# Kernel tuning notes

Measured on AMD Instinct MI355X. Metric: run time of the kernel, lower is better.

## Reference

```python
import jax, jax.numpy as jnp
import numpy as np

TEMPERATURE = 0.07
NEG = -9e15  # matches torch masked_fill value
EPS = 1e-8   # torch.nn.functional.cosine_similarity eps


def setup_inputs() -> dict:
    key = jax.random.key(0)
    k1, k2 = jax.random.split(key)
    B, D = 4096, 512
    return {
        "feats1": jax.random.normal(k1, (B, D), dtype=jnp.float32),
        "feats2": jax.random.normal(k2, (B, D), dtype=jnp.float32),
    }


def reference(feats1, feats2):
    feats = jnp.concatenate([feats1, feats2], axis=0)            # [2N, D]
    n = feats.shape[0]
    # cosine similarity via normalize-once + GEMM (same math as the
    # broadcasted F.cosine_similarity, incl. per-vector eps clamp)
    norms = jnp.maximum(jnp.linalg.norm(feats, axis=-1, keepdims=True), EPS)
    fn = feats / norms                                            # [2N, D]
    cos_sim = fn @ fn.T                                           # [2N, 2N]
    # mask self-similarity BEFORE temperature division (as in torch code)
    idx = jnp.arange(n)
    cos_sim = jnp.where(idx[:, None] == idx[None, :], NEG, cos_sim)
    cos_sim = cos_sim / TEMPERATURE
    # positive pair: eye rolled by N rows -> column (i + N) mod 2N
    pos_idx = (idx + n // 2) % n
    pos = cos_sim[idx, pos_idx]                                   # [2N]
    nll = jnp.mean(-pos + jax.nn.logsumexp(cos_sim, axis=-1))
    # ranking: rank of the positive among [pos, masked negatives];
    # equals # of masked entries strictly greater than pos
    masked = jnp.where(idx[None, :] == pos_idx[:, None], NEG, cos_sim)
    rank = jnp.sum(masked > pos[:, None], axis=-1)                # int [2N]
    acc_top1 = jnp.mean((rank == 0).astype(jnp.float32))
    acc_top5 = jnp.mean((rank < 5).astype(jnp.float32))
    acc_mean_pos = 1.0 + jnp.mean(rank.astype(jnp.float32))
    return (nll, acc_top1, acc_top5, acc_mean_pos)
```

## Files before the change

kernel.cpp:

```cpp
#include <hip/hip_runtime.h>
#include <math.h>
#include <stdint.h>

#define NTOT   8192
#define HALF_N 4096
#define DIM    512
#define INV_T  14.2857142857142857f
#define NTILE  64
#define NBLK   2080

using s16x8 = __attribute__((ext_vector_type(8))) short;
using f32x4 = __attribute__((ext_vector_type(4))) float;

__device__ unsigned short g_fnb[NTOT * DIM];
__device__ float g_pos[NTOT];
__device__ float g_ps[NTILE * NTOT];
__device__ int   g_pc[NTILE * NTOT];
__device__ float g_sumexp[NTOT];
__device__ int   g_cnt[NTOT];

__device__ __forceinline__ float bf2f(unsigned short u) {
  union { unsigned int i; float f; } v; v.i = ((unsigned int)u) << 16; return v.f;
}
__device__ __forceinline__ unsigned short f2bf(float x) {
  union { float f; unsigned int i; } v; v.f = x;
  unsigned int u = v.i;
  return (unsigned short)((u + 0x7FFFu + ((u >> 16) & 1u)) >> 16);
}

__device__ __forceinline__ void gload16(const unsigned short* g, unsigned short* l) {
  __builtin_amdgcn_global_load_lds(
      (const __attribute__((address_space(1))) unsigned int*)g,
      (__attribute__((address_space(3))) unsigned int*)l, 16, 0, 0);
}

__global__ __launch_bounds__(256) void knorm(const float* __restrict__ f1,
                                             const float* __restrict__ f2) {
  const int tid  = threadIdx.x;
  const int wv   = tid >> 6;
  const int pi   = wv >> 1;
  const int half = wv & 1;
  const int lane = tid & 63;
  const int b    = blockIdx.x * 2 + pi;
  const int row  = b + half * HALF_N;

  const float* src = (half == 0) ? (f1 + (size_t)b * DIM) : (f2 + (size_t)b * DIM);
  float4 v0 = ((const float4*)src)[lane];
  float4 v1 = ((const float4*)src)[lane + 64];
  float ss = v0.x*v0.x + v0.y*v0.y + v0.z*v0.z + v0.w*v0.w
           + v1.x*v1.x + v1.y*v1.y + v1.z*v1.z + v1.w*v1.w;
  #pragma unroll
  for (int o = 32; o >= 1; o >>= 1) ss += __shfl_xor(ss, o, 64);
  const float sc = 1.0f / fmaxf(sqrtf(ss), 1e-8f);
  ushort4 h0, h1;
  h0.x = f2bf(v0.x * sc); h0.y = f2bf(v0.y * sc);
  h0.z = f2bf(v0.z * sc); h0.w = f2bf(v0.w * sc);
  h1.x = f2bf(v1.x * sc); h1.y = f2bf(v1.y * sc);
  h1.z = f2bf(v1.z * sc); h1.w = f2bf(v1.w * sc);
  ushort4* dst = (ushort4*)(g_fnb + (size_t)row * DIM);
  dst[lane]      = h0;
  dst[lane + 64] = h1;

  __shared__ ushort4 sh[2][64][2];
  if (half == 1) { sh[pi][lane][0] = h0; sh[pi][lane][1] = h1; }
  __syncthreads();
  if (half == 0) {
    const ushort4 p0 = sh[pi][lane][0], p1 = sh[pi][lane][1];
    float s = bf2f(h0.x)*bf2f(p0.x) + bf2f(h0.y)*bf2f(p0.y)
            + bf2f(h0.z)*bf2f(p0.z) + bf2f(h0.w)*bf2f(p0.w)
            + bf2f(h1.x)*bf2f(p1.x) + bf2f(h1.y)*bf2f(p1.y)
            + bf2f(h1.z)*bf2f(p1.z) + bf2f(h1.w)*bf2f(p1.w);
    #pragma unroll
    for (int o = 32; o >= 1; o >>= 1) s += __shfl_xor(s, o, 64);
    if (lane == 0) { g_pos[b] = s; g_pos[b + HALF_N] = s; }
  }
}

__global__ __launch_bounds__(256, 4) void kmain() {
  __shared__ __align__(16) unsigned short As[128 * 64];
  __shared__ __align__(16) unsigned short Bs[128 * 64];
  __shared__ float sRowS[128]; __shared__ int sRowC[128];
  __shared__ float sColS[128]; __shared__ int sColC[128];

  int t = (blockIdx.x & 7) * (NBLK / 8) + (blockIdx.x >> 3);
  int bi = 0, rem = NTILE;
  while (t >= rem) { t -= rem; --rem; ++bi; }
  const int bj = bi + t;
  const bool offdiag = (bi != bj);
  const int i0 = bi * 128, j0 = bj * 128;

  const int tid  = threadIdx.x;
  const int lane = tid & 63;
  const int w    = tid >> 6;
  const int wr   = (w >> 1) * 64;
  const int wc   = (w & 1) * 64;
  const int lrow = lane & 15;
  const int lq   = lane >> 4;

  const int rsub = lane >> 3;
  const int lcb  = (lane & 7) ^ rsub;
  const unsigned short* Ag = g_fnb + (size_t)(i0 + w * 32 + rsub) * DIM + lcb * 8;
  const unsigned short* Bg = g_fnb + (size_t)(j0 + w * 32 + rsub) * DIM + lcb * 8;
  unsigned short* Al = &As[w * 32 * 64];
  unsigned short* Bl = &Bs[w * 32 * 64];

  f32x4 acc[4][4];
  #pragma unroll
  for (int a = 0; a < 4; ++a)
    #pragma unroll
    for (int bb = 0; bb < 4; ++bb) { acc[a][bb][0]=0.f; acc[a][bb][1]=0.f; acc[a][bb][2]=0.f; acc[a][bb][3]=0.f; }

  const unsigned short* Bls = offdiag ? (const unsigned short*)Bs
                                      : (const unsigned short*)As;

  for (int kt = 0; kt < 8; ++kt) {
    __syncthreads();
    const int kb = kt * 64;
    #pragma unroll
    for (int q = 0; q < 4; ++q) {
      gload16(Ag + (size_t)(q * 8) * DIM + kb, Al + q * 512);
      if (offdiag) gload16(Bg + (size_t)(q * 8) * DIM + kb, Bl + q * 512);
    }
    __syncthreads();

    #pragma unroll
    for (int kk = 0; kk < 2; ++kk) {
      s16x8 af[4], bf[4];
      #pragma unroll
      for (int mi = 0; mi < 4; ++mi) {
        const int r = wr + mi * 16 + lrow;
        af[mi] = *(const s16x8*)(&As[r * 64 + (((kk * 4 + lq) ^ (lrow & 7)) * 8)]);
      }
      #pragma unroll
      for (int ni = 0; ni < 4; ++ni) {
        const int r = wc + ni * 16 + lrow;
        bf[ni] = *(const s16x8*)(&Bls[r * 64 + (((kk * 4 + lq) ^ (lrow & 7)) * 8)]);
      }
      #pragma unroll
      for (int mi = 0; mi < 4; ++mi)
        #pragma unroll
        for (int ni = 0; ni < 4; ++ni)
          acc[mi][ni] = __builtin_amdgcn_mfma_f32_16x16x32_bf16(af[mi], bf[ni], acc[mi][ni], 0, 0, 0);
    }
  }

  if (tid < 128) { sRowS[tid] = 0.f; sRowC[tid] = 0; sColS[tid] = 0.f; sColC[tid] = 0; }
  __syncthreads();

  #pragma unroll
  for (int mi = 0; mi < 4; ++mi) {
    #pragma unroll
    for (int r = 0; r < 4; ++r) {
      const int ridx = wr + mi * 16 + lq * 4 + r;
      const int i  = i0 + ridx;
      const float pv = g_pos[i];
      float s = 0.f; int c = 0;
      #pragma unroll
      for (int ni = 0; ni < 4; ++ni) {
        const int j = j0 + wc + ni * 16 + lrow;
        const float v = acc[mi][ni][r];
        const float e = __expf(v * INV_T);
        const bool diag = (j == i);
        s += diag ? 0.f : e;
        c += (!diag && (j != (i ^ HALF_N)) && (v > pv)) ? 1 : 0;
      }
      #pragma unroll
      for (int o = 1; o < 16; o <<= 1) {
        s += __shfl_xor(s, o, 64);
        c += __shfl_xor(c, o, 64);
      }
      if (lrow == 0) {
        atomicAdd(&sRowS[ridx], s);
        atomicAdd(&sRowC[ridx], c);
      }
    }
  }

  if (offdiag) {
    #pragma unroll
    for (int ni = 0; ni < 4; ++ni) {
      const int cidx = wc + ni * 16 + lrow;
      const int j  = j0 + cidx;
      const float pj = g_pos[j];
      float s = 0.f; int c = 0;
      #pragma unroll
      for (int mi = 0; mi < 4; ++mi) {
        #pragma unroll
        for (int r = 0; r < 4; ++r) {
          const int i = i0 + wr + mi * 16 + lq * 4 + r;
          const float v = acc[mi][ni][r];
          s += __expf(v * INV_T);
          c += ((i != (j ^ HALF_N)) && (v > pj)) ? 1 : 0;
        }
      }
      s += __shfl_xor(s, 16, 64); s += __shfl_xor(s, 32, 64);
      c += __shfl_xor(c, 16, 64); c += __shfl_xor(c, 32, 64);
      if (lq == 0) {
        atomicAdd(&sColS[cidx], s);
        atomicAdd(&sColC[cidx], c);
      }
    }
  }
  __syncthreads();

  if (tid < 128) {
    g_ps[(size_t)bj * NTOT + i0 + tid] = sRowS[tid];
    g_pc[(size_t)bj * NTOT + i0 + tid] = sRowC[tid];
  } else if (offdiag && tid < 256) {
    const int r2 = tid - 128;
    g_ps[(size_t)bi * NTOT + j0 + r2] = sColS[r2];
    g_pc[(size_t)bi * NTOT + j0 + r2] = sColC[r2];
  }
}

__global__ __launch_bounds__(256) void kred() {
  const int i = blockIdx.x * 256 + threadIdx.x;
  float s = 0.f; int c = 0;
  #pragma unroll 8
  for (int sl = 0; sl < NTILE; ++sl) {
    s += g_ps[(size_t)sl * NTOT + i];
    c += g_pc[(size_t)sl * NTOT + i];
  }
  g_sumexp[i] = s;
  g_cnt[i] = c;
}

__global__ __launch_bounds__(1024) void kfin(float* __restrict__ out) {
  const int tid = threadIdx.x;
  float nll = 0.f, t1 = 0.f, t5 = 0.f, mr = 0.f;
  for (int i = tid; i < NTOT; i += 1024) {
    nll += -g_pos[i] * INV_T + logf(g_sumexp[i]);
    const int c = g_cnt[i];
    t1 += (c == 0) ? 1.f : 0.f;
    t5 += (c < 5) ? 1.f : 0.f;
    mr += (float)c;
  }
  #pragma unroll
  for (int o = 32; o >= 1; o >>= 1) {
    nll += __shfl_xor(nll, o, 64);
    t1  += __shfl_xor(t1, o, 64);
    t5  += __shfl_xor(t5, o, 64);
    mr  += __shfl_xor(mr, o, 64);
  }
  __shared__ float red[16][4];
  const int wv = tid >> 6, lane = tid & 63;
  if (lane == 0) { red[wv][0] = nll; red[wv][1] = t1; red[wv][2] = t5; red[wv][3] = mr; }
  __syncthreads();
  if (tid == 0) {
    float a = 0.f, b = 0.f, c = 0.f, d = 0.f;
    for (int k = 0; k < 16; ++k) { a += red[k][0]; b += red[k][1]; c += red[k][2]; d += red[k][3]; }
    out[0] = a / (float)NTOT;
    out[1] = b / (float)NTOT;
    out[2] = c / (float)NTOT;
    out[3] = 1.f + d / (float)NTOT;
  }
}

extern "C" void kernel_launch(void* const* d_in, const int* in_sizes, int n_in,
                              void* d_out, int out_size, void* d_ws, size_t ws_size,
                              hipStream_t stream) {
  const float* f1 = (const float*)d_in[0];
  const float* f2 = (const float*)d_in[1];
  float* out = (float*)d_out;

  knorm<<<dim3(2048), dim3(256), 0, stream>>>(f1, f2);
  kmain<<<dim3(NBLK), dim3(256), 0, stream>>>();
  kred <<<dim3(32),   dim3(256), 0, stream>>>();
  kfin <<<dim3(1),    dim3(1024), 0, stream>>>(out);
}
```

Measured before the change: 157.4 us.

## Fuse reduction and final kernels into GEMM via atomic last-block folding

Removes the separate kred and kfin kernel launches. Each GEMM tile block bumps a per-row-stripe counter, and the last block to finish a stripe sums that stripe's partial sums and counts and writes a per-stripe partial result. A second counter lets the last stripe produce the final outputs. It also changes the tile enumeration to a grouped 4x4 super-tile order for cache locality. The cost is extra atomics and syncthreads in every block, plus a serial tail in whichever block completes each stripe.

```diff
diff --git a/kernel.cpp b/kernel.cpp
--- a/kernel.cpp
+++ b/kernel.cpp
@@ -14,10 +14,15 @@
 
 __device__ unsigned short g_fnb[NTOT * DIM];
 __device__ float g_pos[NTOT];
-__device__ float g_ps[NTILE * NTOT];
-__device__ int   g_pc[NTILE * NTOT];
-__device__ float g_sumexp[NTOT];
-__device__ int   g_cnt[NTOT];
+__device__ float g_ps[(size_t)NTILE * NTOT];
+__device__ int   g_pc[(size_t)NTILE * NTOT];
+__device__ float g_part[NTILE * 4];
+__device__ int   g_tick[NTILE];
+__device__ int   g_tick2;
+
+__constant__ int c_pre[11] = {0,136,392,648,904,1040,1296,1552,1688,1944,2080};
+__constant__ int c_gi[10]  = {0,0,0,0,1,1,1,2,2,3};
+__constant__ int c_gj[10]  = {0,1,2,3,1,2,3,2,3,3};
 
 __device__ __forceinline__ float bf2f(unsigned short u) {
   union { unsigned int i; float f; } v; v.i = ((unsigned int)u) << 16; return v.f;
@@ -43,6 +48,13 @@
   const int lane = tid & 63;
   const int b    = blockIdx.x * 2 + pi;
   const int row  = b + half * HALF_N;
+
+  if (blockIdx.x == 0) {
+    if (tid < NTILE)
+      __hip_atomic_store(&g_tick[tid], 0, __ATOMIC_RELAXED, __HIP_MEMORY_SCOPE_AGENT);
+    else if (tid == NTILE)
+      __hip_atomic_store(&g_tick2, 0, __ATOMIC_RELAXED, __HIP_MEMORY_SCOPE_AGENT);
+  }
 
   const float* src = (half == 0) ? (f1 + (size_t)b * DIM) : (f2 + (size_t)b * DIM);
   float4 v0 = ((const float4*)src)[lane];
@@ -76,16 +88,27 @@
   }
 }
 
-__global__ __launch_bounds__(256, 4) void kmain() {
+__global__ __launch_bounds__(256, 4) void kmain(float* __restrict__ out) {
   __shared__ __align__(16) unsigned short As[128 * 64];
   __shared__ __align__(16) unsigned short Bs[128 * 64];
   __shared__ float sRowS[128]; __shared__ int sRowC[128];
   __shared__ float sColS[128]; __shared__ int sColC[128];
-
-  int t = (blockIdx.x & 7) * (NBLK / 8) + (blockIdx.x >> 3);
-  int bi = 0, rem = NTILE;
-  while (t >= rem) { t -= rem; --rem; ++bi; }
-  const int bj = bi + t;
+  __shared__ int sFold;
+
+  const int t_sw = (blockIdx.x & 7) * (NBLK / 8) + (blockIdx.x >> 3);
+  int sp = 0;
+  while (t_sw >= c_pre[sp + 1]) ++sp;
+  int l = t_sw - c_pre[sp];
+  int lbi, lbj;
+  if (c_gi[sp] == c_gj[sp]) {
+    int r16 = 16; lbi = 0;
+    while (l >= r16) { l -= r16; --r16; ++lbi; }
+    lbj = lbi + l;
+  } else {
+    lbi = l >> 4; lbj = l & 15;
+  }
+  const int bi = c_gi[sp] * 16 + lbi;
+  const int bj = c_gj[sp] * 16 + lbj;
   const bool offdiag = (bi != bj);
   const int i0 = bi * 128, j0 = bj * 128;
 
@@ -211,48 +234,78 @@
     g_ps[(size_t)bi * NTOT + j0 + r2] = sColS[r2];
     g_pc[(size_t)bi * NTOT + j0 + r2] = sColC[r2];
   }
-}
-
-__global__ __launch_bounds__(256) void kred() {
-  const int i = blockIdx.x * 256 + threadIdx.x;
-  float s = 0.f; int c = 0;
-  #pragma unroll 8
-  for (int sl = 0; sl < NTILE; ++sl) {
-    s += g_ps[(size_t)sl * NTOT + i];
-    c += g_pc[(size_t)sl * NTOT + i];
-  }
-  g_sumexp[i] = s;
-  g_cnt[i] = c;
-}
-
-__global__ __launch_bounds__(1024) void kfin(float* __restrict__ out) {
-  const int tid = threadIdx.x;
-  float nll = 0.f, t1 = 0.f, t5 = 0.f, mr = 0.f;
-  for (int i = tid; i < NTOT; i += 1024) {
-    nll += -g_pos[i] * INV_T + logf(g_sumexp[i]);
-    const int c = g_cnt[i];
-    t1 += (c == 0) ? 1.f : 0.f;
-    t5 += (c < 5) ? 1.f : 0.f;
-    mr += (float)c;
-  }
-  #pragma unroll
-  for (int o = 32; o >= 1; o >>= 1) {
-    nll += __shfl_xor(nll, o, 64);
-    t1  += __shfl_xor(t1, o, 64);
-    t5  += __shfl_xor(t5, o, 64);
-    mr  += __shfl_xor(mr, o, 64);
-  }
-  __shared__ float red[16][4];
-  const int wv = tid >> 6, lane = tid & 63;
-  if (lane == 0) { red[wv][0] = nll; red[wv][1] = t1; red[wv][2] = t5; red[wv][3] = mr; }
   __syncthreads();
-  if (tid == 0) {
-    float a = 0.f, b = 0.f, c = 0.f, d = 0.f;
-    for (int k = 0; k < 16; ++k) { a += red[k][0]; b += red[k][1]; c += red[k][2]; d += red[k][3]; }
-    out[0] = a / (float)NTOT;
-    out[1] = b / (float)NTOT;
-    out[2] = c / (float)NTOT;
-    out[3] = 1.f + d / (float)NTOT;
+
+  for (int side = 0; side < 2; ++side) {
+    if (tid == 0) {
+      int f = -1;
+      if (side == 0 || offdiag) {
+        const int s = (side == 0) ? bi : bj;
+        const int old = __hip_atomic_fetch_add(&g_tick[s], 1,
+                            __ATOMIC_ACQ_REL, __HIP_MEMORY_SCOPE_AGENT);
+        if (old == NTILE - 1) f = s;
+      }
+      sFold = f;
+    }
+    __syncthreads();
+    const int s = sFold;
+    if (s >= 0) {
+      __builtin_amdgcn_fence(__ATOMIC_ACQUIRE, "agent");
+      const int hh = tid >> 7;
+      const int rr = tid & 127;
+      const int i  = s * 128 + rr;
+      float fs = 0.f; int fc = 0;
+      const int sl0 = hh * 32;
+      #pragma unroll 8
+      for (int sl = sl0; sl < sl0 + 32; ++sl) {
+        fs += g_ps[(size_t)sl * NTOT + i];
+        fc += g_pc[(size_t)sl * NTOT + i];
+      }
+      if (hh) { sColS[rr] = fs; sColC[rr] = fc; }
+      __syncthreads();
+      float nll = 0.f, t1 = 0.f, t5 = 0.f, mr = 0.f;
+      if (!hh) {
+        const float se = fs + sColS[rr];
+        const int   c  = fc + sColC[rr];
+        nll = -g_pos[i] * INV_T + logf(se);
+        t1 = (c == 0) ? 1.f : 0.f;
+        t5 = (c < 5) ? 1.f : 0.f;
+        mr = (float)c;
+      }
+      #pragma unroll
+      for (int o = 32; o >= 1; o >>= 1) {
+        nll += __shfl_xor(nll, o, 64);
+        t1  += __shfl_xor(t1, o, 64);
+        t5  += __shfl_xor(t5, o, 64);
+        mr  += __shfl_xor(mr, o, 64);
+      }
+      if (tid == 64) { sColS[0] = nll; sColS[1] = t1; sColS[2] = t5; sColS[3] = mr; }
+      __syncthreads();
+      if (tid == 0) {
+        nll += sColS[0]; t1 += sColS[1]; t5 += sColS[2]; mr += sColS[3];
+        g_part[s * 4 + 0] = nll;
+        g_part[s * 4 + 1] = t1;
+        g_part[s * 4 + 2] = t5;
+        g_part[s * 4 + 3] = mr;
+        const int o2 = __hip_atomic_fetch_add(&g_tick2, 1,
+                           __ATOMIC_ACQ_REL, __HIP_MEMORY_SCOPE_AGENT);
+        if (o2 == NTILE - 1) {
+          __builtin_amdgcn_fence(__ATOMIC_ACQUIRE, "agent");
+          float a = 0.f, b = 0.f, cc = 0.f, d = 0.f;
+          for (int k2 = 0; k2 < NTILE; ++k2) {
+            a  += g_part[k2 * 4 + 0];
+            b  += g_part[k2 * 4 + 1];
+            cc += g_part[k2 * 4 + 2];
+            d  += g_part[k2 * 4 + 3];
+          }
+          out[0] = a / (float)NTOT;
+          out[1] = b / (float)NTOT;
+          out[2] = cc / (float)NTOT;
+          out[3] = 1.f + d / (float)NTOT;
+        }
+      }
+    }
+    __syncthreads();
   }
 }
 
@@ -264,7 +317,5 @@
   float* out = (float*)d_out;
 
   knorm<<<dim3(2048), dim3(256), 0, stream>>>(f1, f2);
-  kmain<<<dim3(NBLK), dim3(256), 0, stream>>>();
-  kred <<<dim3(32),   dim3(256), 0, stream>>>();
-  kfin <<<dim3(1),    dim3(1024), 0, stream>>>(out);
-}
+  kmain<<<dim3(NBLK), dim3(256), 0, stream>>>(out);
+}
```

New measurement: 266.8 us. 69.5% more time.
